# Kernel optimization log

Measured on AMD Instinct MI355X. Metric: run time of the kernel, lower is better.

## Reference

```python
import jax, jax.numpy as jnp
import numpy as np

N = 100000      # nodes
E = 1600000     # edges (avg degree 16)
EMB = 64        # embedding_size (per-head out channels)
H = 2           # heads (hardcoded in module)
HID = 128       # hidden_size
NEG_SLOPE = 0.2 # GATv2 default


def setup_inputs() -> dict:
    key = jax.random.key(0)
    ks = jax.random.split(key, 12)
    s = 0.1
    x = jax.random.normal(ks[0], (N, 1), jnp.float32)
    edge_index = jax.random.randint(ks[1], (2, E), 0, N, dtype=jnp.int64)
    edge_attr = jax.random.normal(ks[2], (E, 1), jnp.float32)
    # GATv2Conv params (in_channels=1, out=EMB, heads=H, edge_dim=1)
    W_l = jax.random.normal(ks[3], (1, H * EMB), jnp.float32) * s
    b_l = jnp.zeros((H * EMB,), jnp.float32)
    W_r = jax.random.normal(ks[4], (1, H * EMB), jnp.float32) * s
    b_r = jnp.zeros((H * EMB,), jnp.float32)
    W_e = jax.random.normal(ks[5], (1, H * EMB), jnp.float32) * s   # lin_edge, bias=False
    att = jax.random.normal(ks[6], (H, EMB), jnp.float32) * s       # attention vector a
    bias_out = jnp.zeros((H * EMB,), jnp.float32)                   # conv output bias (concat=True)
    # fc: Linear(embedding_size*4, hidden_size)
    W_fc = jax.random.normal(ks[7], (HID, 4 * EMB), jnp.float32) * s
    b_fc = jnp.zeros((HID,), jnp.float32)
    return {
        "x": x, "edge_index": edge_index, "edge_attr": edge_attr,
        "target_node_idx": 123,
        "W_l": W_l, "b_l": b_l, "W_r": W_r, "b_r": b_r,
        "W_e": W_e, "att": att, "bias_out": bias_out,
        "W_fc": W_fc, "b_fc": b_fc,
    }


def reference(x, edge_index, edge_attr, target_node_idx,
              W_l, b_l, W_r, b_r, W_e, att, bias_out, W_fc, b_fc):
    n = x.shape[0]
    h, c = att.shape
    src, dst = edge_index[0], edge_index[1]

    # add_self_loops with fill_value='mean': per-target-node mean of incoming edge_attr
    deg = jax.ops.segment_sum(jnp.ones((src.shape[0],), x.dtype), dst, num_segments=n)
    attr_mean = jax.ops.segment_sum(edge_attr, dst, num_segments=n) / jnp.maximum(deg, 1.0)[:, None]
    loop = jnp.arange(n, dtype=src.dtype)
    src_f = jnp.concatenate([src, loop])
    dst_f = jnp.concatenate([dst, loop])
    ea = jnp.concatenate([edge_attr, attr_mean], axis=0)  # [E+N, 1]

    # per-head node transforms
    x_l = (x @ W_l + b_l).reshape(n, h, c)  # source transform
    x_r = (x @ W_r + b_r).reshape(n, h, c)  # target transform
    e_edge = (ea @ W_e).reshape(-1, h, c)   # edge-feature transform

    # GATv2: e_ij = a^T LeakyReLU(W_l x_j + W_r x_i + W_e e_ij)
    e = jax.nn.leaky_relu(x_l[src_f] + x_r[dst_f] + e_edge, NEG_SLOPE)  # [E', H, C]
    logits = jnp.einsum('ehc,hc->eh', e, att)  # [E', H]

    # segment softmax over incoming edges per target node
    m = jax.ops.segment_max(logits, dst_f, num_segments=n)     # [N, H]
    expv = jnp.exp(logits - m[dst_f])
    denom = jax.ops.segment_sum(expv, dst_f, num_segments=n)
    alpha = expv / denom[dst_f]                                 # [E', H]

    # weighted scatter-aggregate of source messages, concat heads, add bias
    out = jax.ops.segment_sum(alpha[:, :, None] * x_l[src_f], dst_f, num_segments=n)
    graph_emb = out.reshape(n, h * c) + bias_out                # [N, 2*EMB]

    # gather target, repeat, concat, linear
    tgt = graph_emb[target_node_idx]                            # [2*EMB]
    combined = jnp.concatenate([graph_emb, jnp.broadcast_to(tgt[None, :], graph_emb.shape)], axis=1)
    return combined @ W_fc.T + b_fc                             # [N, HID]
```

## Files before the change

kernel.cpp:

```cpp
#include <hip/hip_runtime.h>
#include <math.h>


#define LRELU_A1 0.6f
#define LRELU_A2 0.4f
#define TB       256
#define EPB      2048
#define NPB      128
#define NB_MAX   1024
#define LUTSZ    2048

__global__ void k_prep(const unsigned int* __restrict__ ei,
                       const float* __restrict__ att,
                       const float* __restrict__ W_l,
                       const float* __restrict__ b_l, const float* __restrict__ b_r,
                       const float* __restrict__ bias_out,
                       const float* __restrict__ W_fc, const float* __restrict__ b_fc,
                       float* __restrict__ C) {
  int j = threadIdx.x;
  unsigned long long nz = __ballot(j < 32 && ei[2 * j + 1] != 0u);
  if (j == 0) ((int*)C)[1024] = (nz == 0ull) ? 1 : 0;
  if (j >= 128) return;
  float a = att[j];
  C[j] = LRELU_A1 * a;
  C[128 + j] = LRELU_A2 * a;
  C[256 + j] = b_l[j] + b_r[j];
  const float* wrow = W_fc + j * 256;
  float u0 = 0.f, u1 = 0.f, v0 = 0.f, v1 = 0.f, cb = b_fc[j];
  for (int c = 0; c < 64; c++) {
    u0 = fmaf(W_l[c],      wrow[c],       u0);
    u1 = fmaf(W_l[64 + c], wrow[64 + c],  u1);
    v0 = fmaf(W_l[c],      wrow[128 + c], v0);
    v1 = fmaf(W_l[64 + c], wrow[192 + c], v1);
  }
  for (int t = 0; t < 128; t++) {
    float gb = b_l[t] + bias_out[t];
    cb = fmaf(gb, wrow[t] + wrow[128 + t], cb);
  }
  C[384 + j] = u0;
  C[512 + j] = u1;
  C[640 + j] = v0;
  C[768 + j] = v1;
  C[896 + j] = cb;
}

#define CH_STEP(comp, ACC, i)                                                      \
  do {                                                                             \
    float v_ = fmaf(xs8[i], wl.comp, fmaf(xt8[i], wr.comp, fmaf(ae8[i], we.comp, bb.comp))); \
    ACC[i] = fmaf(a2.comp, fabsf(v_), fmaf(a1.comp, v_, ACC[i]));                  \
  } while (0)

__global__ __launch_bounds__(TB, 4) void k_bin(
    const float* __restrict__ x, const int* __restrict__ ei,
    const float* __restrict__ ea,
    const float* __restrict__ WL, const float* __restrict__ WR,
    const float* __restrict__ WE, const float* __restrict__ C,
    int4* __restrict__ rec, int* __restrict__ offsT,
    int NB, int S_BLOCKS, int E) {
  __shared__ int cnt[NB_MAX];
  __shared__ int pfx[NB_MAX + 1];
  __shared__ int sc[TB];
  const int tid = threadIdx.x;
  for (int i = tid; i < NB_MAX; i += TB) cnt[i] = 0;
  __syncthreads();

  const int e0 = blockIdx.x * EPB;
  const bool w64 = ((const int*)C)[1024] != 0;
  const float* A1 = C;
  const float* A2 = C + 128;
  const float* BASE = C + 256;

  int de8[8];
  float ae8[8], xs8[8], xt8[8];
  bool ok[8];
#pragma unroll
  for (int i = 0; i < 8; i++) {
    int e = e0 + i * TB + tid;
    ok[i] = (e < E);
    int ee = ok[i] ? e : 0;
    int s_ = w64 ? ei[2 * ee] : ei[ee];
    int d_ = w64 ? ei[2 * (E + ee)] : ei[E + ee];
    de8[i] = d_;
    ae8[i] = ea[ee];
    xs8[i] = x[s_];
    xt8[i] = x[d_];
  }
  float acc0[8] = {0.f, 0.f, 0.f, 0.f, 0.f, 0.f, 0.f, 0.f};
  float acc1[8] = {0.f, 0.f, 0.f, 0.f, 0.f, 0.f, 0.f, 0.f};
#pragma unroll 2
  for (int jb = 0; jb < 64; jb += 4) {
    float4 wl = *(const float4*)(WL + jb);
    float4 wr = *(const float4*)(WR + jb);
    float4 we = *(const float4*)(WE + jb);
    float4 bb = *(const float4*)(BASE + jb);
    float4 a1 = *(const float4*)(A1 + jb);
    float4 a2 = *(const float4*)(A2 + jb);
#pragma unroll
    for (int i = 0; i < 8; i++) {
      CH_STEP(x, acc0, i); CH_STEP(y, acc0, i); CH_STEP(z, acc0, i); CH_STEP(w, acc0, i);
    }
  }
#pragma unroll 2
  for (int jb = 64; jb < 128; jb += 4) {
    float4 wl = *(const float4*)(WL + jb);
    float4 wr = *(const float4*)(WR + jb);
    float4 we = *(const float4*)(WE + jb);
    float4 bb = *(const float4*)(BASE + jb);
    float4 a1 = *(const float4*)(A1 + jb);
    float4 a2 = *(const float4*)(A2 + jb);
#pragma unroll
    for (int i = 0; i < 8; i++) {
      CH_STEP(x, acc1, i); CH_STEP(y, acc1, i); CH_STEP(z, acc1, i); CH_STEP(w, acc1, i);
    }
  }
  int b8[8], slot8[8], p0[8], p1[8], p2[8], p3[8];
#pragma unroll
  for (int i = 0; i < 8; i++) {
    int d_ = de8[i];
    b8[i] = d_ >> 7;
    p0[i] = __float_as_int(__expf(acc0[i]));
    p1[i] = __float_as_int(__expf(acc1[i]));
    p2[i] = __float_as_int(xs8[i]);
    p3[i] = (int)((__float_as_uint(ae8[i]) & ~127u) | (unsigned)(d_ & 127));
    slot8[i] = ok[i] ? atomicAdd(&cnt[b8[i]], 1) : 0;
  }
  __syncthreads();
  int l4[4], mysum = 0;
#pragma unroll
  for (int j = 0; j < 4; j++) {
    int idx = tid * 4 + j;
    l4[j] = (idx < NB) ? cnt[idx] : 0;
    mysum += l4[j];
  }
  sc[tid] = mysum;
  __syncthreads();
  for (int st = 1; st < TB; st <<= 1) {
    int v = (tid >= st) ? sc[tid - st] : 0;
    __syncthreads();
    sc[tid] += v;
    __syncthreads();
  }
  int run = sc[tid] - mysum;
#pragma unroll
  for (int j = 0; j < 4; j++) {
    int idx = tid * 4 + j;
    if (idx < NB) { pfx[idx] = run; run += l4[j]; }
  }
  if (tid == 0) pfx[NB] = sc[TB - 1];
  __syncthreads();
  for (int b = tid; b <= NB; b += TB)
    offsT[(size_t)b * S_BLOCKS + blockIdx.x] = pfx[b];
  int4* myrec = rec + (size_t)blockIdx.x * EPB;
#pragma unroll
  for (int i = 0; i < 8; i++) {
    if (ok[i]) myrec[pfx[b8[i]] + slot8[i]] = make_int4(p0[i], p1[i], p2[i], p3[i]);
  }
}

__global__ __launch_bounds__(TB, 4) void k_reduce(
    const int4* __restrict__ rec, const int* __restrict__ offsT,
    float* __restrict__ Spart, int S_BLOCKS, int SPP) {
  __shared__ float lacc[NPB * 7];
  __shared__ int sc[TB];
  __shared__ int lut[LUTSZ];
  const int tid = threadIdx.x;
  const int b = blockIdx.x;
  const int part = blockIdx.y;
  for (int i = tid; i < NPB * 7; i += TB) lacc[i] = 0.f;

  const int sA = part * SPP + tid;
  const int sB = sA + TB;
  int stA = 0, lenA = 0, stB = 0, lenB = 0;
  if (tid < SPP && sA < S_BLOCKS) {
    stA  = offsT[(size_t)b * S_BLOCKS + sA];
    lenA = offsT[(size_t)(b + 1) * S_BLOCKS + sA] - stA;
  }
  if (TB + tid < SPP && sB < S_BLOCKS) {
    stB  = offsT[(size_t)b * S_BLOCKS + sB];
    lenB = offsT[(size_t)(b + 1) * S_BLOCKS + sB] - stB;
  }
  const int rbA = sA * EPB + stA;
  const int rbB = sB * EPB + stB;
  const int mysum = lenA + lenB;
  sc[tid] = mysum;
  __syncthreads();
  for (int d = 1; d < TB; d <<= 1) {
    int v = (tid >= d) ? sc[tid - d] : 0;
    __syncthreads();
    sc[tid] += v;
    __syncthreads();
  }
  const int T = sc[TB - 1];
  const int bsA = sc[tid] - mysum;
  const int bsB = bsA + lenA;

  for (int w0 = 0; w0 < T; w0 += LUTSZ) {
    const int w1 = min(w0 + LUTSZ, T);
    {
      int lo = max(bsA, w0), hi = min(bsA + lenA, w1);
      for (int k = lo; k < hi; k++) lut[k - w0] = rbA + (k - bsA);
      lo = max(bsB, w0); hi = min(bsB + lenB, w1);
      for (int k = lo; k < hi; k++) lut[k - w0] = rbB + (k - bsB);
    }
    __syncthreads();
    for (int i = w0 + tid; i < w1; i += TB) {
      int4 r = rec[(size_t)(unsigned)lut[i - w0]];
      float e0v = __int_as_float(r.x);
      float e1v = __int_as_float(r.y);
      float xsv = __int_as_float(r.z);
      unsigned eab = (unsigned)r.w;
      float* a = lacc + (int)(eab & 127u) * 7;
      float aev = __uint_as_float(eab & ~127u);
      atomicAdd(a + 0, e0v);
      atomicAdd(a + 1, e0v * xsv);
      atomicAdd(a + 2, e1v);
      atomicAdd(a + 3, e1v * xsv);
      atomicAdd(a + 4, aev);
      atomicAdd(a + 5, 1.0f);
    }
    __syncthreads();
  }
  float* out = Spart + ((size_t)b * gridDim.y + part) * (NPB * 6);
  for (int u = tid; u < NPB * 6; u += TB)
    out[u] = lacc[(u / 6) * 7 + (u % 6)];
}

__global__ __launch_bounds__(256) void k_fin(
    const float* __restrict__ x,
    const float* __restrict__ WL, const float* __restrict__ WR,
    const float* __restrict__ WE, const float* __restrict__ C,
    const float* __restrict__ Spart, float* __restrict__ S,
    int N, int P) {
  int n = blockIdx.x * blockDim.x + threadIdx.x;
  if (n >= N) return;
  int b = n >> 7, t = n & 127;
  const float* q0 = Spart + ((size_t)b * P) * (NPB * 6) + t * 6;
  float den0 = 0.f, num0 = 0.f, den1 = 0.f, num1 = 0.f, asum = 0.f, cntv = 0.f;
  for (int p = 0; p < P; p++) {
    const float* q = q0 + (size_t)p * (NPB * 6);
    float2 v0 = *(const float2*)(q);
    float2 v1 = *(const float2*)(q + 2);
    float2 v2 = *(const float2*)(q + 4);
    den0 += v0.x; num0 += v0.y;
    den1 += v1.x; num1 += v1.y;
    asum += v2.x; cntv += v2.y;
  }
  const float* A1 = C;
  const float* A2 = C + 128;
  const float* BASE = C + 256;
  float xn = x[n];
  float am = asum / fmaxf(cntv, 1.0f);
  float acc0 = 0.f, acc1 = 0.f;
#pragma unroll 4
  for (int jb = 0; jb < 64; jb += 4) {
    float4 wl = *(const float4*)(WL + jb);
    float4 wr = *(const float4*)(WR + jb);
    float4 we = *(const float4*)(WE + jb);
    float4 bb = *(const float4*)(BASE + jb);
    float4 a1 = *(const float4*)(A1 + jb);
    float4 a2 = *(const float4*)(A2 + jb);
    float v;
    v = fmaf(xn, wl.x + wr.x, fmaf(am, we.x, bb.x)); acc0 = fmaf(a2.x, fabsf(v), fmaf(a1.x, v, acc0));
    v = fmaf(xn, wl.y + wr.y, fmaf(am, we.y, bb.y)); acc0 = fmaf(a2.y, fabsf(v), fmaf(a1.y, v, acc0));
    v = fmaf(xn, wl.z + wr.z, fmaf(am, we.z, bb.z)); acc0 = fmaf(a2.z, fabsf(v), fmaf(a1.z, v, acc0));
    v = fmaf(xn, wl.w + wr.w, fmaf(am, we.w, bb.w)); acc0 = fmaf(a2.w, fabsf(v), fmaf(a1.w, v, acc0));
  }
#pragma unroll 4
  for (int jb = 64; jb < 128; jb += 4) {
    float4 wl = *(const float4*)(WL + jb);
    float4 wr = *(const float4*)(WR + jb);
    float4 we = *(const float4*)(WE + jb);
    float4 bb = *(const float4*)(BASE + jb);
    float4 a1 = *(const float4*)(A1 + jb);
    float4 a2 = *(const float4*)(A2 + jb);
    float v;
    v = fmaf(xn, wl.x + wr.x, fmaf(am, we.x, bb.x)); acc1 = fmaf(a2.x, fabsf(v), fmaf(a1.x, v, acc1));
    v = fmaf(xn, wl.y + wr.y, fmaf(am, we.y, bb.y)); acc1 = fmaf(a2.y, fabsf(v), fmaf(a1.y, v, acc1));
    v = fmaf(xn, wl.z + wr.z, fmaf(am, we.z, bb.z)); acc1 = fmaf(a2.z, fabsf(v), fmaf(a1.z, v, acc1));
    v = fmaf(xn, wl.w + wr.w, fmaf(am, we.w, bb.w)); acc1 = fmaf(a2.w, fabsf(v), fmaf(a1.w, v, acc1));
  }
  float s0 = __expf(acc0), s1 = __expf(acc1);
  float2 sv;
  sv.x = (num0 + s0 * xn) / (den0 + s0);
  sv.y = (num1 + s1 * xn) / (den1 + s1);
  *(float2*)(S + 2 * n) = sv;
}

__global__ __launch_bounds__(256) void k_out(
    const float* __restrict__ S, const float* __restrict__ C,
    const int* __restrict__ tgtp, float* __restrict__ out, int N) {
  int g = blockIdx.x * blockDim.x + threadIdx.x;
  if (g >= N * 32) return;
  int n = g >> 5;
  int kq = (g & 31) * 4;
  int T = tgtp[0];
  float s0t = S[2 * T], s1t = S[2 * T + 1];
  float2 s = *(const float2*)(S + 2 * n);
  float4 u0 = *(const float4*)(C + 384 + kq);
  float4 u1 = *(const float4*)(C + 512 + kq);
  float4 v0 = *(const float4*)(C + 640 + kq);
  float4 v1 = *(const float4*)(C + 768 + kq);
  float4 cb = *(const float4*)(C + 896 + kq);
  float4 o;
  o.x = fmaf(s.x, u0.x, fmaf(s.y, u1.x, fmaf(s0t, v0.x, fmaf(s1t, v1.x, cb.x))));
  o.y = fmaf(s.x, u0.y, fmaf(s.y, u1.y, fmaf(s0t, v0.y, fmaf(s1t, v1.y, cb.y))));
  o.z = fmaf(s.x, u0.z, fmaf(s.y, u1.z, fmaf(s0t, v0.z, fmaf(s1t, v1.z, cb.z))));
  o.w = fmaf(s.x, u0.w, fmaf(s.y, u1.w, fmaf(s0t, v0.w, fmaf(s1t, v1.w, cb.w))));
  *(float4*)(out + n * 128 + kq) = o;
}

extern "C" void kernel_launch(void* const* d_in, const int* in_sizes, int n_in,
                              void* d_out, int out_size, void* d_ws, size_t ws_size,
                              hipStream_t stream) {
  const float* x        = (const float*)d_in[0];
  const int*   ei       = (const int*)d_in[1];
  const float* ea       = (const float*)d_in[2];
  const int*   tgt      = (const int*)d_in[3];
  const float* W_l      = (const float*)d_in[4];
  const float* b_l      = (const float*)d_in[5];
  const float* W_r      = (const float*)d_in[6];
  const float* b_r      = (const float*)d_in[7];
  const float* W_e      = (const float*)d_in[8];
  const float* att      = (const float*)d_in[9];
  const float* bias_out = (const float*)d_in[10];
  const float* W_fc     = (const float*)d_in[11];
  const float* b_fc     = (const float*)d_in[12];

  const int N = in_sizes[0];
  const int E = in_sizes[2];
  const int NB = (N + NPB - 1) / NPB;
  const int S_BLOCKS = (E + EPB - 1) / EPB;

  const size_t sz_rec  = (size_t)S_BLOCKS * EPB * 16;
  const size_t sz_offs = (size_t)(NB + 1) * S_BLOCKS * 4;
  const size_t sz_S    = (size_t)2 * N * 4;
  const size_t sz_C    = 4608;
  int P = 4;
  while (P > 2 &&
         sz_rec + sz_offs + sz_S + sz_C + (size_t)NB * P * NPB * 6 * 4 > ws_size)
    P >>= 1;
  const int SPP = (S_BLOCKS + P - 1) / P;

  char* p = (char*)d_ws;
  int4*  rec   = (int4*)p;                      p += sz_rec;
  int*   offsT = (int*)p;                       p += sz_offs;
  float* S     = (float*)p;                     p += sz_S;
  float* C     = (float*)p;                     p += sz_C;
  float* Spart = (float*)p;

  k_prep<<<1, 128, 0, stream>>>((const unsigned int*)ei, att, W_l, b_l, b_r,
                                bias_out, W_fc, b_fc, C);
  k_bin<<<S_BLOCKS, TB, 0, stream>>>(x, ei, ea, W_l, W_r, W_e, C,
                                     rec, offsT, NB, S_BLOCKS, E);
  k_reduce<<<dim3(NB, P), TB, 0, stream>>>(rec, offsT, Spart, S_BLOCKS, SPP);
  k_fin<<<(N + 255) / 256, 256, 0, stream>>>(x, W_l, W_r, W_e, C, Spart, S, N, P);
  k_out<<<(N * 32 + 255) / 256, 256, 0, stream>>>(S, C, tgt, (float*)d_out, N);
}
```

Before: 233.0 us.

## Replace shared-memory float atomics with per-node counting sort and register reduction

The reduce kernel no longer accumulates each edge record into shared memory with six float atomicAdds. Each window of records is counting-sorted by local node: an integer count, a prefix scan, then a scatter into a shared staging buffer. One thread per node then sums its records in registers and writes the partials directly. The window shrinks to 512 records and the partition count P doubles to 8 for more parallelism. The costs are that each record is read from global memory twice, there are extra barriers per window, only half the threads do the summation, and the final k_fin pass must combine more partials.

```diff
diff --git a/kernel.cpp b/kernel.cpp
--- a/kernel.cpp
+++ b/kernel.cpp
@@ -8,7 +8,7 @@
 #define EPB      2048
 #define NPB      128
 #define NB_MAX   1024
-#define LUTSZ    2048
+#define SW       512
 
 __global__ void k_prep(const unsigned int* __restrict__ ei,
                        const float* __restrict__ att,
@@ -160,13 +160,15 @@
 __global__ __launch_bounds__(TB, 4) void k_reduce(
     const int4* __restrict__ rec, const int* __restrict__ offsT,
     float* __restrict__ Spart, int S_BLOCKS, int SPP) {
-  __shared__ float lacc[NPB * 7];
+  __shared__ int4 sorted[SW];
+  __shared__ int lut[SW];
   __shared__ int sc[TB];
-  __shared__ int lut[LUTSZ];
+  __shared__ int cnt[NPB];
+  __shared__ int pos0[NPB];
+  __shared__ int claim[NPB];
   const int tid = threadIdx.x;
   const int b = blockIdx.x;
   const int part = blockIdx.y;
-  for (int i = tid; i < NPB * 7; i += TB) lacc[i] = 0.f;
 
   const int sA = part * SPP + tid;
   const int sB = sA + TB;
@@ -183,6 +185,7 @@
   const int rbB = sB * EPB + stB;
   const int mysum = lenA + lenB;
   sc[tid] = mysum;
+  if (tid < NPB) cnt[tid] = 0;
   __syncthreads();
   for (int d = 1; d < TB; d <<= 1) {
     int v = (tid >= d) ? sc[tid - d] : 0;
@@ -194,8 +197,11 @@
   const int bsA = sc[tid] - mysum;
   const int bsB = bsA + lenA;
 
-  for (int w0 = 0; w0 < T; w0 += LUTSZ) {
-    const int w1 = min(w0 + LUTSZ, T);
+  float r0 = 0.f, r1 = 0.f, r2 = 0.f, r3 = 0.f, r4 = 0.f;
+  int rc = 0;
+
+  for (int w0 = 0; w0 < T; w0 += SW) {
+    const int w1 = min(w0 + SW, T);
     {
       int lo = max(bsA, w0), hi = min(bsA + lenA, w1);
       for (int k = lo; k < hi; k++) lut[k - w0] = rbA + (k - bsA);
@@ -205,24 +211,54 @@
     __syncthreads();
     for (int i = w0 + tid; i < w1; i += TB) {
       int4 r = rec[(size_t)(unsigned)lut[i - w0]];
-      float e0v = __int_as_float(r.x);
-      float e1v = __int_as_float(r.y);
-      float xsv = __int_as_float(r.z);
-      unsigned eab = (unsigned)r.w;
-      float* a = lacc + (int)(eab & 127u) * 7;
-      float aev = __uint_as_float(eab & ~127u);
-      atomicAdd(a + 0, e0v);
-      atomicAdd(a + 1, e0v * xsv);
-      atomicAdd(a + 2, e1v);
-      atomicAdd(a + 3, e1v * xsv);
-      atomicAdd(a + 4, aev);
-      atomicAdd(a + 5, 1.0f);
-    }
-    __syncthreads();
-  }
-  float* out = Spart + ((size_t)b * gridDim.y + part) * (NPB * 6);
-  for (int u = tid; u < NPB * 6; u += TB)
-    out[u] = lacc[(u / 6) * 7 + (u % 6)];
+      atomicAdd(&cnt[(int)((unsigned)r.w & 127u)], 1);
+    }
+    __syncthreads();
+    if (tid < 64) {
+      int c0 = cnt[2 * tid], c1 = cnt[2 * tid + 1];
+      int s = c0 + c1;
+      for (int d = 1; d < 64; d <<= 1) {
+        int t = __shfl_up(s, d);
+        if (tid >= d) s += t;
+      }
+      int excl = s - (c0 + c1);
+      pos0[2 * tid] = excl;
+      pos0[2 * tid + 1] = excl + c0;
+      claim[2 * tid] = excl;
+      claim[2 * tid + 1] = excl + c0;
+    }
+    __syncthreads();
+    for (int i = w0 + tid; i < w1; i += TB) {
+      int4 r = rec[(size_t)(unsigned)lut[i - w0]];
+      int node = (int)((unsigned)r.w & 127u);
+      int slot = atomicAdd(&claim[node], 1);
+      sorted[slot] = r;
+    }
+    __syncthreads();
+    if (tid < NPB) {
+      int p = pos0[tid], c = cnt[tid];
+      for (int k = 0; k < c; k++) {
+        int4 r = sorted[p + k];
+        float e0v = __int_as_float(r.x);
+        float e1v = __int_as_float(r.y);
+        float xsv = __int_as_float(r.z);
+        float aev = __uint_as_float((unsigned)r.w & ~127u);
+        r0 += e0v;
+        r1 += e0v * xsv;
+        r2 += e1v;
+        r3 += e1v * xsv;
+        r4 += aev;
+      }
+      rc += c;
+      cnt[tid] = 0;
+    }
+    __syncthreads();
+  }
+  if (tid < NPB) {
+    float* out = Spart + ((size_t)b * gridDim.y + part) * (NPB * 6) + tid * 6;
+    out[0] = r0; out[1] = r1; out[2] = r2;
+    out[3] = r3; out[4] = r4; out[5] = (float)rc;
+  }
 }
 
 __global__ __launch_bounds__(256) void k_fin(
@@ -335,7 +371,7 @@
   const size_t sz_offs = (size_t)(NB + 1) * S_BLOCKS * 4;
   const size_t sz_S    = (size_t)2 * N * 4;
   const size_t sz_C    = 4608;
-  int P = 4;
+  int P = 8;
   while (P > 2 &&
          sz_rec + sz_offs + sz_S + sz_C + (size_t)NB * P * NPB * 6 * 4 > ws_size)
     P >>= 1;
```

Measured after the change: 207.5 us. 11.0% less time.
